# Kernel optimization log

Measured on AMD Instinct MI355X. Metric: run time of the kernel, lower is better.

The kernel has to match this reference:

```python
import jax, jax.numpy as jnp
import numpy as np

B, S, D_MODEL, H = 4, 2048, 1024, 16
DEPTH = D_MODEL // H          # 64
HD = DEPTH // 2               # 32, per-head projection dim
SCALE = float(np.sqrt(DEPTH))  # note: sqrt(full depth), as in the torch code
NEG = -1e10


def setup_inputs() -> dict:
    key = jax.random.key(0)
    kq, kk, kv, km, kwq, kwk, kwv, kwo = jax.random.split(key, 8)
    q = jax.random.normal(kq, (B, S, D_MODEL), dtype=jnp.float32)
    k = jax.random.normal(kk, (B, S, D_MODEL), dtype=jnp.float32)
    v = jax.random.normal(kv, (B, S, D_MODEL), dtype=jnp.float32)
    attention_mask = jax.random.uniform(km, (B, S, S)) < 0.1
    # xavier-uniform-ish init; stacked per-head weights [H, d_model, hd]
    lim_qkv = float(np.sqrt(6.0 / (D_MODEL + HD)))
    Wq = jax.random.uniform(kwq, (H, D_MODEL, HD), minval=-lim_qkv, maxval=lim_qkv)
    Wk = jax.random.uniform(kwk, (H, D_MODEL, HD), minval=-lim_qkv, maxval=lim_qkv)
    Wv = jax.random.uniform(kwv, (H, D_MODEL, HD), minval=-lim_qkv, maxval=lim_qkv)
    lim_o = float(np.sqrt(6.0 / (H * HD + D_MODEL)))
    Wo = jax.random.uniform(kwo, (H * HD, D_MODEL), minval=-lim_o, maxval=lim_o)
    return {"q": q, "k": k, "v": v, "attention_mask": attention_mask,
            "Wq": Wq, "Wk": Wk, "Wv": Wv, "Wo": Wo}


def reference(q, k, v, attention_mask, Wq, Wk, Wv, Wo):
    # batched per-head projections (equivalent to the per-head Linear loop)
    Q = jnp.einsum('bsd,hde->bhse', q, Wq)   # [B,H,S,hd]
    K = jnp.einsum('bsd,hde->bhse', k, Wk)
    V = jnp.einsum('bsd,hde->bhse', v, Wv)
    scores = jnp.einsum('bhqe,bhke->bhqk', Q, K) / SCALE  # [B,H,S,S]
    scores = jnp.where(attention_mask[:, None, :, :], NEG, scores)
    attn = jax.nn.softmax(scores, axis=-1)
    z = jnp.einsum('bhqk,bhke->bhqe', attn, V)            # [B,H,S,hd]
    # concat heads along last dim (head order matches torch cat)
    multi = z.transpose(0, 2, 1, 3).reshape(q.shape[0], q.shape[1], H * HD)
    out = multi @ Wo                                       # [B,S,d_model]
    return out  # dropout p=0.0 (eval) is identity
```

## Files before the change

kernel.cpp:

```cpp
#include <hip/hip_runtime.h>
#include <hip/hip_bf16.h>
#include <math.h>

typedef unsigned short u16;
typedef unsigned int u32;
typedef unsigned long long u64;
typedef __attribute__((ext_vector_type(8))) short s16x8;
typedef __attribute__((ext_vector_type(4))) short s16x4;
typedef __attribute__((ext_vector_type(4))) float f32x4;
typedef __attribute__((ext_vector_type(16))) float f32x16;
typedef __attribute__((ext_vector_type(2))) unsigned int u32x2;

#define DEV static __device__ __forceinline__

DEV u16 f2bf(float f){
  __hip_bfloat16 h = __float2bfloat16(f);
  return *reinterpret_cast<u16*>(&h);
}

DEV u32 cvt_pk_bf16(float lo, float hi_){
  u32 r;
  asm("v_cvt_pk_bf16_f32 %0, %1, %2" : "=v"(r) : "v"(lo), "v"(hi_));
  return r;
}

DEV u32x2 pl32swap(u32 a, u32 b){
  return __builtin_amdgcn_permlane32_swap(a, b, false, false);
}
DEV float xhalf_sum(float x){
  u32x2 r = pl32swap(__float_as_uint(x), __float_as_uint(x));
  return __uint_as_float(r[0]) + __uint_as_float(r[1]);
}

template<int CPOS> DEV float mzero(float p, u32 msn){
  int ext;
  asm("v_bfe_i32 %0, %1, %2, 1" : "=v"(ext) : "v"(msn), "n"(CPOS));
  return __uint_as_float(__float_as_uint(p) & (u32)ext);
}

__global__ void detect_mask_kernel(const unsigned char* __restrict__ m, int* __restrict__ flag){
  __shared__ int cnt;
  if (threadIdx.x==0) cnt=0;
  __syncthreads();
  int nz=0;
  for (int i=threadIdx.x;i<4096;i+=256) nz += (m[(size_t)i*4+1]!=0)?1:0;
  if (nz) atomicAdd(&cnt, nz);
  __syncthreads();
  if (threadIdx.x==0) *flag = (cnt==0)?4:1;
}

__global__ __launch_bounds__(256) void pack_mask_kernel(const unsigned char* __restrict__ m,
    const int* __restrict__ flag, u16* __restrict__ mb16){
  const int stride = *flag;
  const size_t gid = (size_t)blockIdx.x*256u + threadIdx.x;
  u32 bits = 0;
  if (stride == 1){
    const uint4 v = *(const uint4*)(m + gid*16);
    bits  =  ((v.x & 0x01010101u) * 0x01020408u) >> 24;
    bits |= (((v.y & 0x01010101u) * 0x01020408u) >> 24) << 4;
    bits |= (((v.z & 0x01010101u) * 0x01020408u) >> 24) << 8;
    bits |= (((v.w & 0x01010101u) * 0x01020408u) >> 24) << 12;
  } else {
    const unsigned char* mm = m + gid*64;
    const uint4 a = *(const uint4*)(mm);
    const uint4 b = *(const uint4*)(mm+16);
    const uint4 c = *(const uint4*)(mm+32);
    const uint4 d = *(const uint4*)(mm+48);
    bits  = (u32)(a.x!=0) | ((u32)(a.y!=0)<<1) | ((u32)(a.z!=0)<<2) | ((u32)(a.w!=0)<<3)
          | ((u32)(b.x!=0)<<4) | ((u32)(b.y!=0)<<5) | ((u32)(b.z!=0)<<6) | ((u32)(b.w!=0)<<7)
          | ((u32)(c.x!=0)<<8) | ((u32)(c.y!=0)<<9) | ((u32)(c.z!=0)<<10)| ((u32)(c.w!=0)<<11)
          | ((u32)(d.x!=0)<<12)| ((u32)(d.y!=0)<<13)| ((u32)(d.z!=0)<<14)| ((u32)(d.w!=0)<<15);
  }
  mb16[gid] = (u16)bits;
}

__global__ __launch_bounds__(256) void prep_weights_kernel(
    const float* __restrict__ Wq, const float* __restrict__ Wk, const float* __restrict__ Wv,
    const float* __restrict__ Wo, u16* __restrict__ WT, u16* __restrict__ WoT){
  int gid = blockIdx.x*256 + threadIdx.x;
  if (gid < 3*512*1024){
    int z = gid >> 19;
    int r = gid & ((1<<19)-1);
    int n = r >> 10, d = r & 1023;
    const float* W = (z==0)?Wq:((z==1)?Wk:Wv);
    int h = n>>5, e = n&31;
    float wv = W[((size_t)h*1024 + (size_t)d)*32 + e];
    if (z==0) wv *= 0.18033688011112042f;
    WT[gid] = f2bf(wv);
  } else {
    int r = gid - 3*512*1024;
    int n = r >> 9, cc = r & 511;
    WoT[r] = f2bf(Wo[(size_t)cc*1024 + n]);
  }
}

__global__ __launch_bounds__(256) void gemm_proj_kernel(
    const float* __restrict__ Aq, const float* __restrict__ Ak, const float* __restrict__ Av,
    const u16* __restrict__ WT, u16* __restrict__ Qp, u16* __restrict__ Kp, u16* __restrict__ Vt)
{
  __shared__ u16 As[128*64];
  __shared__ u16 Bs[128*64];
  const int z = blockIdx.z;
  const float* __restrict__ A = (z==0)?Aq:((z==1)?Ak:Av);
  const u16* __restrict__ W = WT + (size_t)z*(512*1024);
  const int m0 = blockIdx.x*128, n0 = blockIdx.y*128;
  const int t = threadIdx.x, lane = t&63, wv = t>>6;
  const int wr = wv>>1, wc = wv&1;
  const int c = lane&15, g = lane>>4;
  f32x4 acc[4][4] = {};
  for (int kk=0; kk<1024; kk+=64){
    #pragma unroll
    for (int j=0;j<8;j++){
      int idx = t + j*256;
      int row = idx>>4, kq=(idx&15)<<2;
      f32x4 a4 = *(const f32x4*)(A + (size_t)(m0+row)*1024 + kk + kq);
      s16x4 b4;
      b4[0]=(short)f2bf(a4[0]); b4[1]=(short)f2bf(a4[1]);
      b4[2]=(short)f2bf(a4[2]); b4[3]=(short)f2bf(a4[3]);
      int co = (kq<<1) ^ ((row&7)<<4);
      *(s16x4*)((char*)As + row*128 + co) = b4;
    }
    #pragma unroll
    for (int j=0;j<4;j++){
      int idx = t + j*256;
      int n = idx>>3, k8=(idx&7)<<3;
      s16x8 bv = *(const s16x8*)(W + (size_t)(n0+n)*1024 + kk + k8);
      int co = (k8<<1) ^ ((n&7)<<4);
      *(s16x8*)((char*)Bs + n*128 + co) = bv;
    }
    __syncthreads();
    #pragma unroll
    for (int ks=0;ks<2;ks++){
      s16x8 af[4], bf[4];
      #pragma unroll
      for (int i=0;i<4;i++){
        int ra = wr*64 + i*16 + c;
        af[i] = *(const s16x8*)((const char*)As + ra*128 + ((ks*64 + g*16) ^ ((ra&7)<<4)));
        int rb = wc*64 + i*16 + c;
        bf[i] = *(const s16x8*)((const char*)Bs + rb*128 + ((ks*64 + g*16) ^ ((rb&7)<<4)));
      }
      #pragma unroll
      for (int mi=0;mi<4;mi++)
        #pragma unroll
        for (int nj=0;nj<4;nj++)
          acc[mi][nj] = __builtin_amdgcn_mfma_f32_16x16x32_bf16(af[mi], bf[nj], acc[mi][nj], 0, 0, 0);
    }
    __syncthreads();
  }
  #pragma unroll
  for (int mi=0;mi<4;mi++){
    #pragma unroll
    for (int nj=0;nj<4;nj++){
      #pragma unroll
      for (int r=0;r<4;r++){
        int gm = m0 + wr*64 + mi*16 + g*4 + r;
        int gn = n0 + wc*64 + nj*16 + c;
        u16 val = f2bf(acc[mi][nj][r]);
        int b = gm>>11, s = gm&2047, hh = gn>>5, e = gn&31;
        if (z==0)      Qp[((size_t)(b*16+hh)*2048 + s)*32 + e] = val;
        else if (z==1) Kp[((size_t)(b*16+hh)*2048 + s)*32 + e] = val;
        else           Vt[((size_t)(b*16+hh)*32 + e)*2048 + s] = val;
      }
    }
  }
}

__global__ __launch_bounds__(256, 4) void attn_kernel(
    const u16* __restrict__ Qp, const u16* __restrict__ Kp, const u16* __restrict__ Vt,
    const u32* __restrict__ mb32, u16* __restrict__ Z)
{
  __shared__ float Psh[2][32][33];
  __shared__ float Tsh[2][32][33];
  __shared__ float Lsh[2][32];
  const int t = threadIdx.x, lane = t&63, wid = t>>6;
  const int c = lane&31, hi = lane>>5;
  const int hi8 = hi*8;
  const int qt = wid>>1, kh = wid&1;
  const int wg = blockIdx.x;
  const int xcd = wg & 7, loc = wg >> 3;
  const int bh = xcd*8 + (loc>>5);
  const int qg = loc & 31;
  const int b = bh>>4, h = bh&15;
  const int q0 = qg*64 + qt*32;
  const u16* Qh = Qp + (size_t)bh*2048*32;
  const u16* Kh = Kp + (size_t)bh*2048*32;
  const u16* Vh = Vt + (size_t)bh*32*2048;

  const s16x8 qf0 = *(const s16x8*)(Qh + (size_t)(q0 + c)*32 + hi8);
  const s16x8 qf1 = *(const s16x8*)(Qh + (size_t)(q0 + c)*32 + 16 + hi8);

  const f32x16 z16 = {0,0,0,0,0,0,0,0,0,0,0,0,0,0,0,0};
  f32x16 OA = z16, OB = z16;
  f32x4 LA = {0,0,0,0}, LB = {0,0,0,0};
  const u32* mrowp = mb32 + ((size_t)b*2048 + (size_t)(q0 + c))*64;
  const int kt0 = kh*32;

  for (int kt = kt0; kt < kt0 + 32; kt += 2){
    const int kbA = kt*32, kbB = kbA + 32;
    const u16* kbaseA = Kh + (size_t)(kbA + c)*32 + hi8;
    const s16x8 kfA0 = *(const s16x8*)(kbaseA);
    const s16x8 kfA1 = *(const s16x8*)(kbaseA + 16);
    const u16* kbaseB = Kh + (size_t)(kbB + c)*32 + hi8;
    const s16x8 kfB0 = *(const s16x8*)(kbaseB);
    const s16x8 kfB1 = *(const s16x8*)(kbaseB + 16);
    const u16* vbase = Vh + (size_t)c*2048 + kbA + hi8;
    const s16x8 vfA0 = *(const s16x8*)(vbase);
    const s16x8 vfA1 = *(const s16x8*)(vbase + 16);
    const s16x8 vfB0 = *(const s16x8*)(vbase + 32);
    const s16x8 vfB1 = *(const s16x8*)(vbase + 48);
    const u64 mw = *(const u64*)(mrowp + kt);
    const u32 msnA = ~(((u32)mw) >> (4*hi));
    const u32 msnB = ~(((u32)(mw >> 32)) >> (4*hi));

    f32x16 pA = __builtin_amdgcn_mfma_f32_32x32x16_bf16(kfA0, qf0, z16, 0, 0, 0);
    pA = __builtin_amdgcn_mfma_f32_32x32x16_bf16(kfA1, qf1, pA, 0, 0, 0);
    f32x16 pB = __builtin_amdgcn_mfma_f32_32x32x16_bf16(kfB0, qf0, z16, 0, 0, 0);
    pB = __builtin_amdgcn_mfma_f32_32x32x16_bf16(kfB1, qf1, pB, 0, 0, 0);

    #define MZE(P,R,MS) P[R] = mzero<(((R)&3)+8*((R)>>2))>(__builtin_amdgcn_exp2f(P[R]), MS)
    MZE(pA,0,msnA);  MZE(pA,1,msnA);  MZE(pA,2,msnA);  MZE(pA,3,msnA);
    MZE(pA,4,msnA);  MZE(pA,5,msnA);  MZE(pA,6,msnA);  MZE(pA,7,msnA);
    MZE(pA,8,msnA);  MZE(pA,9,msnA);  MZE(pA,10,msnA); MZE(pA,11,msnA);
    MZE(pA,12,msnA); MZE(pA,13,msnA); MZE(pA,14,msnA); MZE(pA,15,msnA);
    MZE(pB,0,msnB);  MZE(pB,1,msnB);  MZE(pB,2,msnB);  MZE(pB,3,msnB);
    MZE(pB,4,msnB);  MZE(pB,5,msnB);  MZE(pB,6,msnB);  MZE(pB,7,msnB);
    MZE(pB,8,msnB);  MZE(pB,9,msnB);  MZE(pB,10,msnB); MZE(pB,11,msnB);
    MZE(pB,12,msnB); MZE(pB,13,msnB); MZE(pB,14,msnB); MZE(pB,15,msnB);
    #undef MZE

    #pragma unroll
    for (int i=0;i<4;i++){
      LA[i] += (pA[i] + pA[i+4]) + (pA[i+8] + pA[i+12]);
      LB[i] += (pB[i] + pB[i+4]) + (pB[i+8] + pB[i+12]);
    }

    u32 pwA0 = cvt_pk_bf16(pA[0],  pA[1]);
    u32 pwA1 = cvt_pk_bf16(pA[2],  pA[3]);
    u32 pwA2 = cvt_pk_bf16(pA[4],  pA[5]);
    u32 pwA3 = cvt_pk_bf16(pA[6],  pA[7]);
    u32 pwA4 = cvt_pk_bf16(pA[8],  pA[9]);
    u32 pwA5 = cvt_pk_bf16(pA[10], pA[11]);
    u32 pwA6 = cvt_pk_bf16(pA[12], pA[13]);
    u32 pwA7 = cvt_pk_bf16(pA[14], pA[15]);
    u32x2 a02 = pl32swap(pwA0, pwA2);
    u32x2 a13 = pl32swap(pwA1, pwA3);
    u32x2 a46 = pl32swap(pwA4, pwA6);
    u32x2 a57 = pl32swap(pwA5, pwA7);
    union { u32 u[4]; s16x8 v; } fA0 = {{a02[0], a13[0], a02[1], a13[1]}};
    union { u32 u[4]; s16x8 v; } fA1 = {{a46[0], a57[0], a46[1], a57[1]}};
    u32 pwB0 = cvt_pk_bf16(pB[0],  pB[1]);
    u32 pwB1 = cvt_pk_bf16(pB[2],  pB[3]);
    u32 pwB2 = cvt_pk_bf16(pB[4],  pB[5]);
    u32 pwB3 = cvt_pk_bf16(pB[6],  pB[7]);
    u32 pwB4 = cvt_pk_bf16(pB[8],  pB[9]);
    u32 pwB5 = cvt_pk_bf16(pB[10], pB[11]);
    u32 pwB6 = cvt_pk_bf16(pB[12], pB[13]);
    u32 pwB7 = cvt_pk_bf16(pB[14], pB[15]);
    u32x2 b02 = pl32swap(pwB0, pwB2);
    u32x2 b13 = pl32swap(pwB1, pwB3);
    u32x2 b46 = pl32swap(pwB4, pwB6);
    u32x2 b57 = pl32swap(pwB5, pwB7);
    union { u32 u[4]; s16x8 v; } fB0 = {{b02[0], b13[0], b02[1], b13[1]}};
    union { u32 u[4]; s16x8 v; } fB1 = {{b46[0], b57[0], b46[1], b57[1]}};

    OA = __builtin_amdgcn_mfma_f32_32x32x16_bf16(vfA0, fA0.v, OA, 0, 0, 0);
    OA = __builtin_amdgcn_mfma_f32_32x32x16_bf16(vfA1, fA1.v, OA, 0, 0, 0);
    OB = __builtin_amdgcn_mfma_f32_32x32x16_bf16(vfB0, fB0.v, OB, 0, 0, 0);
    OB = __builtin_amdgcn_mfma_f32_32x32x16_bf16(vfB1, fB1.v, OB, 0, 0, 0);
  }

  const float lown = ((LA[0]+LB[0]) + (LA[1]+LB[1])) + ((LA[2]+LB[2]) + (LA[3]+LB[3]));
  if (kh == 1){
    #pragma unroll
    for (int r=0;r<16;r++){
      const int hd = (r&3) + 8*(r>>2) + 4*hi;
      Psh[qt][c][hd] = OA[r] + OB[r];
    }
    const float s1 = xhalf_sum(lown);
    if (hi == 0) Lsh[qt][c] = s1;
  }
  __syncthreads();
  if (kh == 0){
    const float linv = 1.0f / (xhalf_sum(lown) + Lsh[qt][c]);
    #pragma unroll
    for (int r=0;r<16;r++){
      const int hd = (r&3) + 8*(r>>2) + 4*hi;
      Tsh[qt][c][hd] = ((OA[r] + OB[r]) + Psh[qt][c][hd]) * linv;
    }
  }
  __syncthreads();
  if (kh == 0){
    const int rq = lane >> 1, rc0 = (lane & 1)*16;
    const float* orow = &Tsh[qt][rq][0];
    union { u16 q[8]; s16x8 v; } o0, o1;
    #pragma unroll
    for (int j=0;j<8;j++){ o0.q[j] = f2bf(orow[rc0+j]); o1.q[j] = f2bf(orow[rc0+8+j]); }
    u16* zp = Z + ((size_t)b*2048 + (size_t)(q0 + rq))*512 + h*32 + rc0;
    *(s16x8*)(zp)   = o0.v;
    *(s16x8*)(zp+8) = o1.v;
  }
}

__global__ __launch_bounds__(256) void gemm_out_kernel(
    const u16* __restrict__ Zb, const u16* __restrict__ WoT, float* __restrict__ out)
{
  __shared__ u16 As[128*64];
  __shared__ u16 Bs[128*64];
  const int m0 = blockIdx.x*128, n0 = blockIdx.y*128;
  const int t = threadIdx.x, lane=t&63, wv=t>>6;
  const int wr=wv>>1, wc=wv&1, c=lane&15, g=lane>>4;
  f32x4 acc[4][4] = {};
  for (int kk=0; kk<512; kk+=64){
    #pragma unroll
    for (int j=0;j<4;j++){
      int idx = t + j*256;
      int row = idx>>3, k8=(idx&7)<<3;
      int co = (k8<<1) ^ ((row&7)<<4);
      s16x8 av = *(const s16x8*)(Zb + (size_t)(m0+row)*512 + kk + k8);
      *(s16x8*)((char*)As + row*128 + co) = av;
      s16x8 bv = *(const s16x8*)(WoT + (size_t)(n0+row)*512 + kk + k8);
      *(s16x8*)((char*)Bs + row*128 + co) = bv;
    }
    __syncthreads();
    #pragma unroll
    for (int ks=0;ks<2;ks++){
      s16x8 af[4], bf[4];
      #pragma unroll
      for (int i=0;i<4;i++){
        int ra = wr*64 + i*16 + c;
        af[i] = *(const s16x8*)((const char*)As + ra*128 + ((ks*64 + g*16) ^ ((ra&7)<<4)));
        int rb = wc*64 + i*16 + c;
        bf[i] = *(const s16x8*)((const char*)Bs + rb*128 + ((ks*64 + g*16) ^ ((rb&7)<<4)));
      }
      #pragma unroll
      for (int mi=0;mi<4;mi++)
        #pragma unroll
        for (int nj=0;nj<4;nj++)
          acc[mi][nj] = __builtin_amdgcn_mfma_f32_16x16x32_bf16(af[mi], bf[nj], acc[mi][nj], 0, 0, 0);
    }
    __syncthreads();
  }
  #pragma unroll
  for (int mi=0;mi<4;mi++)
    #pragma unroll
    for (int nj=0;nj<4;nj++)
      #pragma unroll
      for (int r=0;r<4;r++){
        int gm = m0 + wr*64 + mi*16 + g*4 + r;
        int gn = n0 + wc*64 + nj*16 + c;
        out[(size_t)gm*1024 + gn] = acc[mi][nj][r];
      }
}

extern "C" void kernel_launch(void* const* d_in, const int* in_sizes, int n_in,
                              void* d_out, int out_size, void* d_ws, size_t ws_size,
                              hipStream_t stream)
{
  const float* q  = (const float*)d_in[0];
  const float* k  = (const float*)d_in[1];
  const float* v  = (const float*)d_in[2];
  const unsigned char* mask = (const unsigned char*)d_in[3];
  const float* Wq = (const float*)d_in[4];
  const float* Wk = (const float*)d_in[5];
  const float* Wv = (const float*)d_in[6];
  const float* Wo = (const float*)d_in[7];
  float* out = (float*)d_out;

  char* ws = (char*)d_ws;
  u16* Qp  = (u16*)(ws);
  u16* Kp  = (u16*)(ws + 8388608);
  u16* Vt  = (u16*)(ws + 16777216);
  u16* Z   = (u16*)(ws + 25165824);
  u16* WT  = (u16*)(ws + 33554432);
  u16* WoT = (u16*)(ws + 36700160);
  u16* mb16 = (u16*)(ws + 37748736);
  int* flag = (int*)(ws + 39845888);

  detect_mask_kernel<<<1, 256, 0, stream>>>(mask, flag);
  pack_mask_kernel<<<4096, 256, 0, stream>>>(mask, flag, mb16);
  prep_weights_kernel<<<8192, 256, 0, stream>>>(Wq, Wk, Wv, Wo, WT, WoT);
  gemm_proj_kernel<<<dim3(64,4,3), 256, 0, stream>>>(q, k, v, WT, Qp, Kp, Vt);
  attn_kernel<<<2048, 256, 0, stream>>>(Qp, Kp, Vt, (const u32*)mb16, Z);
  gemm_out_kernel<<<dim3(64,8), 256, 0, stream>>>(Z, WoT, out);
  (void)in_sizes; (void)n_in; (void)out_size; (void)ws_size;
}
```

Baseline: 214.4 us.

## Process two query tiles per wave in attention to reuse K/V fragments

```diff
diff --git a/kernel.cpp b/kernel.cpp
--- a/kernel.cpp
+++ b/kernel.cpp
@@ -169,53 +169,51 @@
     const u16* __restrict__ Qp, const u16* __restrict__ Kp, const u16* __restrict__ Vt,
     const u32* __restrict__ mb32, u16* __restrict__ Z)
 {
-  __shared__ float Psh[2][32][33];
-  __shared__ float Tsh[2][32][33];
-  __shared__ float Lsh[2][32];
+  __shared__ float Psh[2][2][32][33];
+  __shared__ float Lsh[2][2][32];
   const int t = threadIdx.x, lane = t&63, wid = t>>6;
   const int c = lane&31, hi = lane>>5;
   const int hi8 = hi*8;
   const int qt = wid>>1, kh = wid&1;
   const int wg = blockIdx.x;
   const int xcd = wg & 7, loc = wg >> 3;
-  const int bh = xcd*8 + (loc>>5);
-  const int qg = loc & 31;
+  const int bh = xcd*8 + (loc>>4);
+  const int qg = loc & 15;
   const int b = bh>>4, h = bh&15;
-  const int q0 = qg*64 + qt*32;
+  const int q0 = qg*128 + qt*64;
   const u16* Qh = Qp + (size_t)bh*2048*32;
   const u16* Kh = Kp + (size_t)bh*2048*32;
   const u16* Vh = Vt + (size_t)bh*32*2048;
 
-  const s16x8 qf0 = *(const s16x8*)(Qh + (size_t)(q0 + c)*32 + hi8);
-  const s16x8 qf1 = *(const s16x8*)(Qh + (size_t)(q0 + c)*32 + 16 + hi8);
+  const s16x8 qfA0 = *(const s16x8*)(Qh + (size_t)(q0 + c)*32 + hi8);
+  const s16x8 qfA1 = *(const s16x8*)(Qh + (size_t)(q0 + c)*32 + 16 + hi8);
+  const s16x8 qfB0 = *(const s16x8*)(Qh + (size_t)(q0 + 32 + c)*32 + hi8);
+  const s16x8 qfB1 = *(const s16x8*)(Qh + (size_t)(q0 + 32 + c)*32 + 16 + hi8);
 
   const f32x16 z16 = {0,0,0,0,0,0,0,0,0,0,0,0,0,0,0,0};
   f32x16 OA = z16, OB = z16;
   f32x4 LA = {0,0,0,0}, LB = {0,0,0,0};
-  const u32* mrowp = mb32 + ((size_t)b*2048 + (size_t)(q0 + c))*64;
+  const u32* mrowpA = mb32 + ((size_t)b*2048 + (size_t)(q0 + c))*64;
+  const u32* mrowpB = mb32 + ((size_t)b*2048 + (size_t)(q0 + 32 + c))*64;
   const int kt0 = kh*32;
 
-  for (int kt = kt0; kt < kt0 + 32; kt += 2){
-    const int kbA = kt*32, kbB = kbA + 32;
-    const u16* kbaseA = Kh + (size_t)(kbA + c)*32 + hi8;
-    const s16x8 kfA0 = *(const s16x8*)(kbaseA);
-    const s16x8 kfA1 = *(const s16x8*)(kbaseA + 16);
-    const u16* kbaseB = Kh + (size_t)(kbB + c)*32 + hi8;
-    const s16x8 kfB0 = *(const s16x8*)(kbaseB);
-    const s16x8 kfB1 = *(const s16x8*)(kbaseB + 16);
-    const u16* vbase = Vh + (size_t)c*2048 + kbA + hi8;
-    const s16x8 vfA0 = *(const s16x8*)(vbase);
-    const s16x8 vfA1 = *(const s16x8*)(vbase + 16);
-    const s16x8 vfB0 = *(const s16x8*)(vbase + 32);
-    const s16x8 vfB1 = *(const s16x8*)(vbase + 48);
-    const u64 mw = *(const u64*)(mrowp + kt);
-    const u32 msnA = ~(((u32)mw) >> (4*hi));
-    const u32 msnB = ~(((u32)(mw >> 32)) >> (4*hi));
-
-    f32x16 pA = __builtin_amdgcn_mfma_f32_32x32x16_bf16(kfA0, qf0, z16, 0, 0, 0);
-    pA = __builtin_amdgcn_mfma_f32_32x32x16_bf16(kfA1, qf1, pA, 0, 0, 0);
-    f32x16 pB = __builtin_amdgcn_mfma_f32_32x32x16_bf16(kfB0, qf0, z16, 0, 0, 0);
-    pB = __builtin_amdgcn_mfma_f32_32x32x16_bf16(kfB1, qf1, pB, 0, 0, 0);
+  #pragma unroll 2
+  for (int i = 0; i < 32; ++i){
+    const int kt = kt0 + i;
+    const int kb = kt*32;
+    const u16* kbase = Kh + (size_t)(kb + c)*32 + hi8;
+    const s16x8 kf0 = *(const s16x8*)(kbase);
+    const s16x8 kf1 = *(const s16x8*)(kbase + 16);
+    const u16* vbase = Vh + (size_t)c*2048 + kb + hi8;
+    const s16x8 vf0 = *(const s16x8*)(vbase);
+    const s16x8 vf1 = *(const s16x8*)(vbase + 16);
+    const u32 msnA = ~(mrowpA[kt] >> (4*hi));
+    const u32 msnB = ~(mrowpB[kt] >> (4*hi));
+
+    f32x16 pA = __builtin_amdgcn_mfma_f32_32x32x16_bf16(kf0, qfA0, z16, 0, 0, 0);
+    pA = __builtin_amdgcn_mfma_f32_32x32x16_bf16(kf1, qfA1, pA, 0, 0, 0);
+    f32x16 pB = __builtin_amdgcn_mfma_f32_32x32x16_bf16(kf0, qfB0, z16, 0, 0, 0);
+    pB = __builtin_amdgcn_mfma_f32_32x32x16_bf16(kf1, qfB1, pB, 0, 0, 0);
 
     #define MZE(P,R,MS) P[R] = mzero<(((R)&3)+8*((R)>>2))>(__builtin_amdgcn_exp2f(P[R]), MS)
     MZE(pA,0,msnA);  MZE(pA,1,msnA);  MZE(pA,2,msnA);  MZE(pA,3,msnA);
@@ -229,9 +227,9 @@
     #undef MZE
 
     #pragma unroll
-    for (int i=0;i<4;i++){
-      LA[i] += (pA[i] + pA[i+4]) + (pA[i+8] + pA[i+12]);
-      LB[i] += (pB[i] + pB[i+4]) + (pB[i+8] + pB[i+12]);
+    for (int u=0;u<4;u++){
+      LA[u] += (pA[u] + pA[u+4]) + (pA[u+8] + pA[u+12]);
+      LB[u] += (pB[u] + pB[u+4]) + (pB[u+8] + pB[u+12]);
     }
 
     u32 pwA0 = cvt_pk_bf16(pA[0],  pA[1]);
@@ -263,41 +261,53 @@
     union { u32 u[4]; s16x8 v; } fB0 = {{b02[0], b13[0], b02[1], b13[1]}};
     union { u32 u[4]; s16x8 v; } fB1 = {{b46[0], b57[0], b46[1], b57[1]}};
 
-    OA = __builtin_amdgcn_mfma_f32_32x32x16_bf16(vfA0, fA0.v, OA, 0, 0, 0);
-    OA = __builtin_amdgcn_mfma_f32_32x32x16_bf16(vfA1, fA1.v, OA, 0, 0, 0);
-    OB = __builtin_amdgcn_mfma_f32_32x32x16_bf16(vfB0, fB0.v, OB, 0, 0, 0);
-    OB = __builtin_amdgcn_mfma_f32_32x32x16_bf16(vfB1, fB1.v, OB, 0, 0, 0);
-  }
-
-  const float lown = ((LA[0]+LB[0]) + (LA[1]+LB[1])) + ((LA[2]+LB[2]) + (LA[3]+LB[3]));
+    OA = __builtin_amdgcn_mfma_f32_32x32x16_bf16(vf0, fA0.v, OA, 0, 0, 0);
+    OA = __builtin_amdgcn_mfma_f32_32x32x16_bf16(vf1, fA1.v, OA, 0, 0, 0);
+    OB = __builtin_amdgcn_mfma_f32_32x32x16_bf16(vf0, fB0.v, OB, 0, 0, 0);
+    OB = __builtin_amdgcn_mfma_f32_32x32x16_bf16(vf1, fB1.v, OB, 0, 0, 0);
+  }
+
+  const float lownA = (LA[0] + LA[1]) + (LA[2] + LA[3]);
+  const float lownB = (LB[0] + LB[1]) + (LB[2] + LB[3]);
   if (kh == 1){
     #pragma unroll
     for (int r=0;r<16;r++){
       const int hd = (r&3) + 8*(r>>2) + 4*hi;
-      Psh[qt][c][hd] = OA[r] + OB[r];
-    }
-    const float s1 = xhalf_sum(lown);
-    if (hi == 0) Lsh[qt][c] = s1;
+      Psh[qt][0][c][hd] = OA[r];
+      Psh[qt][1][c][hd] = OB[r];
+    }
+    const float sA = xhalf_sum(lownA);
+    const float sB = xhalf_sum(lownB);
+    if (hi == 0){ Lsh[qt][0][c] = sA; Lsh[qt][1][c] = sB; }
   }
   __syncthreads();
   if (kh == 0){
-    const float linv = 1.0f / (xhalf_sum(lown) + Lsh[qt][c]);
+    const float linvA = 1.0f / (xhalf_sum(lownA) + Lsh[qt][0][c]);
+    const float linvB = 1.0f / (xhalf_sum(lownB) + Lsh[qt][1][c]);
     #pragma unroll
     for (int r=0;r<16;r++){
       const int hd = (r&3) + 8*(r>>2) + 4*hi;
-      Tsh[qt][c][hd] = ((OA[r] + OB[r]) + Psh[qt][c][hd]) * linv;
+      Psh[qt][0][c][hd] = (OA[r] + Psh[qt][0][c][hd]) * linvA;
+      Psh[qt][1][c][hd] = (OB[r] + Psh[qt][1][c][hd]) * linvB;
     }
   }
   __syncthreads();
   if (kh == 0){
     const int rq = lane >> 1, rc0 = (lane & 1)*16;
-    const float* orow = &Tsh[qt][rq][0];
-    union { u16 q[8]; s16x8 v; } o0, o1;
-    #pragma unroll
-    for (int j=0;j<8;j++){ o0.q[j] = f2bf(orow[rc0+j]); o1.q[j] = f2bf(orow[rc0+8+j]); }
-    u16* zp = Z + ((size_t)b*2048 + (size_t)(q0 + rq))*512 + h*32 + rc0;
-    *(s16x8*)(zp)   = o0.v;
-    *(s16x8*)(zp+8) = o1.v;
+    const float* rowA = &Psh[qt][0][rq][0];
+    const float* rowB = &Psh[qt][1][rq][0];
+    union { u16 q[8]; s16x8 v; } a0, a1, b0, b1;
+    #pragma unroll
+    for (int j=0;j<8;j++){
+      a0.q[j] = f2bf(rowA[rc0+j]); a1.q[j] = f2bf(rowA[rc0+8+j]);
+      b0.q[j] = f2bf(rowB[rc0+j]); b1.q[j] = f2bf(rowB[rc0+8+j]);
+    }
+    u16* zpA = Z + ((size_t)b*2048 + (size_t)(q0 + rq))*512 + h*32 + rc0;
+    u16* zpB = Z + ((size_t)b*2048 + (size_t)(q0 + 32 + rq))*512 + h*32 + rc0;
+    *(s16x8*)(zpA)   = a0.v;
+    *(s16x8*)(zpA+8) = a1.v;
+    *(s16x8*)(zpB)   = b0.v;
+    *(s16x8*)(zpB+8) = b1.v;
   }
 }
 
@@ -380,7 +390,7 @@
   pack_mask_kernel<<<4096, 256, 0, stream>>>(mask, flag, mb16);
   prep_weights_kernel<<<8192, 256, 0, stream>>>(Wq, Wk, Wv, Wo, WT, WoT);
   gemm_proj_kernel<<<dim3(64,4,3), 256, 0, stream>>>(q, k, v, WT, Qp, Kp, Vt);
-  attn_kernel<<<2048, 256, 0, stream>>>(Qp, Kp, Vt, (const u32*)mb16, Z);
+  attn_kernel<<<1024, 256, 0, stream>>>(Qp, Kp, Vt, (const u32*)mb16, Z);
   gemm_out_kernel<<<dim3(64,8), 256, 0, stream>>>(Z, WoT, out);
   (void)in_sizes; (void)n_in; (void)out_size; (void)ws_size;
 }
```

New measurement: 280.9 us. 31.0% more time.
